# Kernel optimization log

Measured on AMD Instinct MI355X. Metric: run time of the kernel, lower is better.

Reference implementation:

```python
import jax, jax.numpy as jnp
import numpy as np

B, H, W, C = 8, 256, 256, 64
M1, M2 = 16, 16
WIDTH = 64
W_SCALE = 0.02  # mimics he-normal-ish init magnitude for complex spectral weights


def setup_inputs() -> dict:
    key = jax.random.key(0)
    k1, k2, k3 = jax.random.split(key, 3)
    x = jax.random.normal(k1, (B, H, W, C), dtype=jnp.float32)
    w_real = jax.random.normal(k2, (M1, M2, C, WIDTH), dtype=jnp.float32)
    w_imag = jax.random.normal(k3, (M1, M2, C, WIDTH), dtype=jnp.float32)
    return {"x": x, "w_real": w_real, "w_imag": w_imag}


def reference(x, w_real, w_imag):
    # complex spectral weights: (M1, M2, C_in, C_out)
    weights = (w_real + 1j * w_imag) * W_SCALE
    spatial = x.shape[1:-1]  # (H, W)
    # full real FFT over spatial axes -> (B, H, W//2+1, C) complex
    x_ft = jnp.fft.rfftn(x, axes=(1, 2))
    # truncate to low-frequency modes
    x_m = x_ft[:, :M1, :M2, :]  # (B, M1, M2, C)
    # per-mode channel mixing (broadcast-ellipsis einsum in the original)
    out_m = jnp.einsum("bxyi,xyio->bxyo", x_m, weights)  # (B, M1, M2, WIDTH)
    # zero-pad back to full spectral grid
    pad = ((0, 0), (0, x_ft.shape[1] - M1), (0, x_ft.shape[2] - M2), (0, 0))
    out_ft = jnp.pad(out_m, pad, mode="constant")
    # inverse real FFT back to spatial domain
    out = jnp.fft.irfftn(out_ft, s=spatial, axes=(1, 2))  # (B, H, W, WIDTH)
    return out
```

## Files before the change

### kernel.cpp

```cpp
#include <hip/hip_runtime.h>


#define NB 8
#define NH 256
#define NW 256
#define NC 64
#define NM 16
#define NO 64

__global__ __launch_bounds__(256) void k_dft_w(const float* __restrict__ x,
                                               float* __restrict__ Gr, float* __restrict__ Gi) {
  __shared__ float2 cs[256];
  const int t = threadIdx.x;
  {
    float s, c;
    sincospif((float)t * (1.0f / 128.0f), &s, &c);
    cs[t] = make_float2(c, s);
  }
  __syncthreads();
  const int b = blockIdx.x >> 7;
  const int h2 = blockIdx.x & 127;
  const int i4 = t & 15;
  const int hs = (t >> 4) & 1;
  const int kyq = t >> 5;
  const int ky0 = kyq * 2, ky1 = ky0 + 1;
  const int h = h2 * 2 + hs;
  const float* xp = x + ((size_t)(b * NH + h) * NW) * NC + i4 * 4;

  float4 ar0 = {0, 0, 0, 0}, ai0 = {0, 0, 0, 0}, ar1 = {0, 0, 0, 0}, ai1 = {0, 0, 0, 0};
  const float2 s0 = cs[ky0], s1 = cs[ky1];
  const float s0r = s0.x, s0i = -s0.y, s1r = s1.x, s1i = -s1.y;

  for (int wc = 0; wc < 8; ++wc) {
    const int w0 = wc * 32;
    const float2 v0 = cs[(ky0 * w0) & 255], v1 = cs[(ky1 * w0) & 255];
    float t0r = v0.x, t0i = -v0.y, t1r = v1.x, t1i = -v1.y;
#pragma unroll 8
    for (int w = 0; w < 32; ++w) {
      const float4 xv = *(const float4*)(xp + (size_t)(w0 + w) * NC);
      ar0.x += t0r * xv.x; ar0.y += t0r * xv.y; ar0.z += t0r * xv.z; ar0.w += t0r * xv.w;
      ai0.x += t0i * xv.x; ai0.y += t0i * xv.y; ai0.z += t0i * xv.z; ai0.w += t0i * xv.w;
      ar1.x += t1r * xv.x; ar1.y += t1r * xv.y; ar1.z += t1r * xv.z; ar1.w += t1r * xv.w;
      ai1.x += t1i * xv.x; ai1.y += t1i * xv.y; ai1.z += t1i * xv.z; ai1.w += t1i * xv.w;
      float n0r = t0r * s0r - t0i * s0i, n0i = t0r * s0i + t0i * s0r;
      float n1r = t1r * s1r - t1i * s1i, n1i = t1r * s1i + t1i * s1r;
      t0r = n0r; t0i = n0i; t1r = n1r; t1i = n1i;
    }
  }
  const size_t g0 = ((size_t)(b * NM + ky0) * NH + h) * NC + i4 * 4;
  const size_t g1 = ((size_t)(b * NM + ky1) * NH + h) * NC + i4 * 4;
  *(float4*)(Gr + g0) = ar0; *(float4*)(Gi + g0) = ai0;
  *(float4*)(Gr + g1) = ar1; *(float4*)(Gi + g1) = ai1;
}

__global__ __launch_bounds__(256) void k_dft_h(const float* __restrict__ Gr, const float* __restrict__ Gi,
                                               float* __restrict__ Xpr, float* __restrict__ Xpi) {
  __shared__ float2 cs[256];
  __shared__ float gr[32 * 64];
  __shared__ float gi[32 * 64];
  const int t = threadIdx.x;
  {
    float s, c;
    sincospif((float)t * (1.0f / 128.0f), &s, &c);
    cs[t] = make_float2(c, s);
  }
  const int b = blockIdx.x >> 7;
  const int ky = (blockIdx.x >> 3) & 15;
  const int hc = blockIdx.x & 7;
  const float* grs = Gr + ((size_t)(b * NM + ky) * NH + hc * 32) * NC;
  const float* gis = Gi + ((size_t)(b * NM + ky) * NH + hc * 32) * NC;
#pragma unroll
  for (int r = 0; r < 2; ++r) {
    ((float4*)gr)[r * 256 + t] = ((const float4*)grs)[r * 256 + t];
    ((float4*)gi)[r * 256 + t] = ((const float4*)gis)[r * 256 + t];
  }
  __syncthreads();
  const int i4 = t & 15;
  const int kx = t >> 4;
  float4 xr = {0, 0, 0, 0}, xi = {0, 0, 0, 0};
  const float2 sv = cs[kx];
  const float str = sv.x, sti = -sv.y;
  const float2 tv = cs[(kx * hc * 32) & 255];
  float twr = tv.x, twi = -tv.y;
#pragma unroll 4
  for (int hh = 0; hh < 32; ++hh) {
    const float4 g_r = *(const float4*)&gr[hh * 64 + i4 * 4];
    const float4 g_i = *(const float4*)&gi[hh * 64 + i4 * 4];
    xr.x += twr * g_r.x - twi * g_i.x;
    xr.y += twr * g_r.y - twi * g_i.y;
    xr.z += twr * g_r.z - twi * g_i.z;
    xr.w += twr * g_r.w - twi * g_i.w;
    xi.x += twr * g_i.x + twi * g_r.x;
    xi.y += twr * g_i.y + twi * g_r.y;
    xi.z += twr * g_i.z + twi * g_r.z;
    xi.w += twr * g_i.w + twi * g_r.w;
    const float nr = twr * str - twi * sti;
    const float ni = twr * sti + twi * str;
    twr = nr; twi = ni;
  }
  const size_t o = ((size_t)((hc * NM + kx) * NM + ky) * NB + b) * NC + i4 * 4;
  *(float4*)(Xpr + o) = xr;
  *(float4*)(Xpi + o) = xi;
}

__global__ __launch_bounds__(256) void k_mix(const float* __restrict__ Xpr, const float* __restrict__ Xpi,
                                             const float* __restrict__ w_real, const float* __restrict__ w_imag,
                                             float2* __restrict__ om) {
  __shared__ float wr_s[64 * 32];
  __shared__ float wi_s[64 * 32];
  __shared__ float2 xc[8 * 64];
  const int t = threadIdx.x;
  const int kx = blockIdx.x >> 5;
  const int ky = (blockIdx.x >> 1) & 15;
  const int oh = blockIdx.x & 1;
  const size_t wb = (size_t)(kx * NM + ky) * 4096 + oh * 32;
#pragma unroll
  for (int r = 0; r < 2; ++r) {
    const int idx = r * 256 + t;
    const int i = idx >> 3, f = idx & 7;
    *(float4*)&wr_s[i * 32 + f * 4] = *(const float4*)(w_real + wb + (size_t)i * 64 + f * 4);
    *(float4*)&wi_s[i * 32 + f * 4] = *(const float4*)(w_imag + wb + (size_t)i * 64 + f * 4);
  }
#pragma unroll
  for (int r = 0; r < 2; ++r) {
    const int idx = r * 256 + t;
    const size_t base = (size_t)(kx * NM + ky) * 512 + idx;
    float sr = 0.f, si = 0.f;
#pragma unroll
    for (int hc = 0; hc < 8; ++hc) {
      sr += Xpr[base + (size_t)hc * 131072];
      si += Xpi[base + (size_t)hc * 131072];
    }
    xc[idx] = make_float2(sr, si);
  }
  __syncthreads();
  const int o = t & 31;
  const int b = t >> 5;
  float r0 = 0.f, i0 = 0.f;
#pragma unroll 8
  for (int i = 0; i < 64; ++i) {
    const float2 xv = xc[b * 64 + i];
    const float wrv = wr_s[i * 32 + o];
    const float wiv = wi_s[i * 32 + o];
    r0 += xv.x * wrv - xv.y * wiv;
    i0 += xv.x * wiv + xv.y * wrv;
  }
  const float sc = (ky == 0 ? 1.0f : 2.0f) * (0.02f / 65536.0f);
  om[((size_t)(b * NM + kx) * NM + ky) * NO + oh * 32 + o] = make_float2(r0 * sc, i0 * sc);
}

__global__ __launch_bounds__(256) void k_idft_w(const float2* __restrict__ om, float2* __restrict__ Zc) {
  __shared__ float2 cs[256];
  const int t = threadIdx.x;
  {
    float s, c;
    sincospif((float)t * (1.0f / 128.0f), &s, &c);
    cs[t] = make_float2(c, s);
  }
  __syncthreads();
  const int b = blockIdx.x >> 7;
  const int kx = (blockIdx.x >> 3) & 15;
  const int wq = blockIdx.x & 7;
  const int o = t & 63;
  const int wg = t >> 6;
  float mr[16], mi[16];
  const size_t base = ((size_t)(b * NM + kx) * NM) * NO + o;
#pragma unroll
  for (int ky = 0; ky < NM; ++ky) {
    const float2 v = om[base + ky * NO];
    mr[ky] = v.x; mi[ky] = v.y;
  }
#pragma unroll
  for (int j = 0; j < 8; ++j) {
    const int w = wq * 32 + wg * 8 + j;
    const float2 st = cs[w];
    float twr = 1.0f, twi = 0.0f;
    float zr = 0.0f, zi = 0.0f;
#pragma unroll
    for (int ky = 0; ky < NM; ++ky) {
      zr += twr * mr[ky] - twi * mi[ky];
      zi += twr * mi[ky] + twi * mr[ky];
      const float nr = twr * st.x - twi * st.y;
      const float ni = twr * st.y + twi * st.x;
      twr = nr; twi = ni;
    }
    Zc[((size_t)(b * NW + w) * NM + kx) * NO + o] = make_float2(zr, zi);
  }
}

__global__ __launch_bounds__(256) void k_idft_h(const float2* __restrict__ Zc, float* __restrict__ out) {
  __shared__ float2 cs[256];
  __shared__ float zre[16 * 64];
  __shared__ float zim[16 * 64];
  const int t = threadIdx.x;
  {
    float s, c;
    sincospif((float)t * (1.0f / 128.0f), &s, &c);
    cs[t] = make_float2(c, s);
  }
  const int b = blockIdx.x >> 9;
  const int w = (blockIdx.x >> 1) & 255;
  const int hh = blockIdx.x & 1;
  const float4* src = (const float4*)(Zc + (size_t)(b * NW + w) * (NM * NO));
#pragma unroll
  for (int r = 0; r < 2; ++r) {
    const int idx = r * 256 + t;
    const float4 v = src[idx];
    ((float2*)zre)[idx] = make_float2(v.x, v.z);
    ((float2*)zim)[idx] = make_float2(v.y, v.w);
  }
  __syncthreads();
  const int i4 = t & 15;
  const int hg = t >> 4;
  const int h0 = hh * 128 + hg * 8;
  float4 acc[8];
#pragma unroll
  for (int j = 0; j < 8; ++j) acc[j] = make_float4(0, 0, 0, 0);
#pragma unroll 4
  for (int kx = 0; kx < 16; ++kx) {
    const float4 zr4 = ((const float4*)zre)[kx * 16 + i4];
    const float4 zi4 = ((const float4*)zim)[kx * 16 + i4];
    const float2 t0 = cs[(kx * h0) & 255];
    const float2 st = cs[kx];
    float twr = t0.x, twi = t0.y;
#pragma unroll
    for (int j = 0; j < 8; ++j) {
      acc[j].x += twr * zr4.x - twi * zi4.x;
      acc[j].y += twr * zr4.y - twi * zi4.y;
      acc[j].z += twr * zr4.z - twi * zi4.z;
      acc[j].w += twr * zr4.w - twi * zi4.w;
      const float nr = twr * st.x - twi * st.y;
      const float ni = twr * st.y + twi * st.x;
      twr = nr; twi = ni;
    }
  }
  float* ob = out + (((size_t)(b * NH) + h0) * NW + w) * NO + i4 * 4;
#pragma unroll
  for (int j = 0; j < 8; ++j) {
    *(float4*)(ob + (size_t)j * (NW * NO)) = acc[j];
  }
}

extern "C" void kernel_launch(void* const* d_in, const int* in_sizes, int n_in,
                              void* d_out, int out_size, void* d_ws, size_t ws_size,
                              hipStream_t stream) {
  const float* x = (const float*)d_in[0];
  const float* w_real = (const float*)d_in[1];
  const float* w_imag = (const float*)d_in[2];
  float* out = (float*)d_out;
  char* ws = (char*)d_ws;

  float* Gr = (float*)(ws);
  float* Gi = (float*)(ws + 8388608);
  float* Xpr = (float*)(ws + 16777216);
  float* Xpi = (float*)(ws + 20971520);
  float2* om = (float2*)(ws + 25165824);
  float2* Zc = (float2*)(ws);

  k_dft_w<<<dim3(1024), dim3(256), 0, stream>>>(x, Gr, Gi);
  k_dft_h<<<dim3(1024), dim3(256), 0, stream>>>(Gr, Gi, Xpr, Xpi);
  k_mix<<<dim3(512), dim3(256), 0, stream>>>(Xpr, Xpi, w_real, w_imag, om);
  k_idft_w<<<dim3(1024), dim3(256), 0, stream>>>(om, Zc);
  k_idft_h<<<dim3(4096), dim3(256), 0, stream>>>(Zc, out);
}
```

Before: 311.5 us.

## Fuse inverse W-DFT into inverse H-DFT kernel, dropping Zc intermediate

Merges the separate inverse DFT along W into the final inverse-H kernel. Each block now computes its 16x64 complex slice for one w directly from the mode-mixed spectrum into shared memory, then runs the H transform. This removes a kernel launch and the global write and read of the Zc intermediate (about 8 MB). In exchange, the W-direction work is recomputed per half-H block, so each value is computed twice, and om is read redundantly. It also raises the unroll factor in the forward H-DFT loop.

```diff
diff --git a/kernel.cpp b/kernel.cpp
--- a/kernel.cpp
+++ b/kernel.cpp
@@ -82,7 +82,7 @@
   const float str = sv.x, sti = -sv.y;
   const float2 tv = cs[(kx * hc * 32) & 255];
   float twr = tv.x, twi = -tv.y;
-#pragma unroll 4
+#pragma unroll 8
   for (int hh = 0; hh < 32; ++hh) {
     const float4 g_r = *(const float4*)&gr[hh * 64 + i4 * 4];
     const float4 g_i = *(const float4*)&gi[hh * 64 + i4 * 4];
@@ -149,8 +149,10 @@
   om[((size_t)(b * NM + kx) * NM + ky) * NO + oh * 32 + o] = make_float2(r0 * sc, i0 * sc);
 }
 
-__global__ __launch_bounds__(256) void k_idft_w(const float2* __restrict__ om, float2* __restrict__ Zc) {
+__global__ __launch_bounds__(256) void k_idft_we(const float2* __restrict__ om, float* __restrict__ out) {
   __shared__ float2 cs[256];
+  __shared__ float zre[16 * 64];
+  __shared__ float zim[16 * 64];
   const int t = threadIdx.x;
   {
     float s, c;
@@ -158,58 +160,34 @@
     cs[t] = make_float2(c, s);
   }
   __syncthreads();
-  const int b = blockIdx.x >> 7;
-  const int kx = (blockIdx.x >> 3) & 15;
-  const int wq = blockIdx.x & 7;
-  const int o = t & 63;
-  const int wg = t >> 6;
-  float mr[16], mi[16];
-  const size_t base = ((size_t)(b * NM + kx) * NM) * NO + o;
-#pragma unroll
-  for (int ky = 0; ky < NM; ++ky) {
-    const float2 v = om[base + ky * NO];
-    mr[ky] = v.x; mi[ky] = v.y;
-  }
-#pragma unroll
-  for (int j = 0; j < 8; ++j) {
-    const int w = wq * 32 + wg * 8 + j;
+  const int b = blockIdx.x >> 9;
+  const int w = (blockIdx.x >> 1) & 255;
+  const int hh = blockIdx.x & 1;
+
+  {
+    const int kx = t >> 4;
+    const int o0 = (t & 15) * 4;
+    const float* ob = (const float*)(om + ((size_t)(b * NM + kx) * NM) * NO + o0);
     const float2 st = cs[w];
     float twr = 1.0f, twi = 0.0f;
-    float zr = 0.0f, zi = 0.0f;
+    float4 zr = {0, 0, 0, 0}, zi = {0, 0, 0, 0};
 #pragma unroll
     for (int ky = 0; ky < NM; ++ky) {
-      zr += twr * mr[ky] - twi * mi[ky];
-      zi += twr * mi[ky] + twi * mr[ky];
+      const float4 A = *(const float4*)(ob + (size_t)ky * 128);
+      const float4 Bv = *(const float4*)(ob + (size_t)ky * 128 + 4);
+      zr.x += twr * A.x - twi * A.y;   zi.x += twr * A.y + twi * A.x;
+      zr.y += twr * A.z - twi * A.w;   zi.y += twr * A.w + twi * A.z;
+      zr.z += twr * Bv.x - twi * Bv.y; zi.z += twr * Bv.y + twi * Bv.x;
+      zr.w += twr * Bv.z - twi * Bv.w; zi.w += twr * Bv.w + twi * Bv.z;
       const float nr = twr * st.x - twi * st.y;
       const float ni = twr * st.y + twi * st.x;
       twr = nr; twi = ni;
     }
-    Zc[((size_t)(b * NW + w) * NM + kx) * NO + o] = make_float2(zr, zi);
-  }
-}
-
-__global__ __launch_bounds__(256) void k_idft_h(const float2* __restrict__ Zc, float* __restrict__ out) {
-  __shared__ float2 cs[256];
-  __shared__ float zre[16 * 64];
-  __shared__ float zim[16 * 64];
-  const int t = threadIdx.x;
-  {
-    float s, c;
-    sincospif((float)t * (1.0f / 128.0f), &s, &c);
-    cs[t] = make_float2(c, s);
-  }
-  const int b = blockIdx.x >> 9;
-  const int w = (blockIdx.x >> 1) & 255;
-  const int hh = blockIdx.x & 1;
-  const float4* src = (const float4*)(Zc + (size_t)(b * NW + w) * (NM * NO));
-#pragma unroll
-  for (int r = 0; r < 2; ++r) {
-    const int idx = r * 256 + t;
-    const float4 v = src[idx];
-    ((float2*)zre)[idx] = make_float2(v.x, v.z);
-    ((float2*)zim)[idx] = make_float2(v.y, v.w);
-  }
-  __syncthreads();
+    *(float4*)&zre[kx * 64 + o0] = zr;
+    *(float4*)&zim[kx * 64 + o0] = zi;
+  }
+  __syncthreads();
+
   const int i4 = t & 15;
   const int hg = t >> 4;
   const int h0 = hh * 128 + hg * 8;
@@ -255,11 +233,9 @@
   float* Xpr = (float*)(ws + 16777216);
   float* Xpi = (float*)(ws + 20971520);
   float2* om = (float2*)(ws + 25165824);
-  float2* Zc = (float2*)(ws);
 
   k_dft_w<<<dim3(1024), dim3(256), 0, stream>>>(x, Gr, Gi);
   k_dft_h<<<dim3(1024), dim3(256), 0, stream>>>(Gr, Gi, Xpr, Xpi);
   k_mix<<<dim3(512), dim3(256), 0, stream>>>(Xpr, Xpi, w_real, w_imag, om);
-  k_idft_w<<<dim3(1024), dim3(256), 0, stream>>>(om, Zc);
-  k_idft_h<<<dim3(4096), dim3(256), 0, stream>>>(Zc, out);
-}
+  k_idft_we<<<dim3(4096), dim3(256), 0, stream>>>(om, out);
+}
```

Measured after the change: 323.1 us. 1.04x slower.
